# Kernel optimization log

Hardware: AMD Instinct MI355X
Metric: run time of the kernel (lower is better)

## Reference

```python
import jax, jax.numpy as jnp
import numpy as np

B, N, D = 64, 2048, 256
EPS = 1e-05


def setup_inputs() -> dict:
    key = jax.random.key(0)
    k1, k2 = jax.random.split(key)
    x = jax.random.normal(k1, (B, N, D), dtype=jnp.float32)
    lengths = jax.random.randint(k2, (B,), 1, N + 1, dtype=jnp.int32)
    weights = jnp.ones((D,), dtype=jnp.float32)
    biases = jnp.zeros((D,), dtype=jnp.float32)
    return {"x": x, "lengths": lengths, "weights": weights, "biases": biases}


def reference(x, lengths, weights, biases):
    # mask: [B, N, 1], 1.0 for valid set elements (idx < length)
    mask = (jnp.arange(N)[None, :] < lengths[:, None])[..., None].astype(x.dtype)
    denom = (lengths.astype(x.dtype) * D)  # [B]
    xm = x * mask
    means = jnp.sum(xm, axis=(1, 2)) / denom                      # [B]
    x_centered = (xm - means[:, None, None]) * mask               # [B,N,D]
    variances = jnp.sum(x_centered * x_centered, axis=(1, 2)) / denom  # [B]
    x_norm = x_centered / (jnp.sqrt(variances)[:, None, None] + EPS)
    # F.linear(x, diag_embed(w), b) == x * w + b (elementwise per-feature affine)
    out = (x_norm * weights + biases) * mask
    return out
```

## Files before the change

### kernel.cpp

```cpp
#include <hip/hip_runtime.h>


#define BB 64
#define NN 2048
#define DD 256
#define EPSV 1e-5f
#define CHUNKS 32
#define GROUPS (NN / 4)
#define BAT4 (NN * DD / 4)
#define K2_BPB 128

typedef float f32x4 __attribute__((ext_vector_type(4)));

__global__ __launch_bounds__(256) void setnorm_pass1(
    const float* __restrict__ x, const int* __restrict__ lengths,
    float* __restrict__ partials, float* __restrict__ out) {
  const int c = blockIdx.x;
  const int b = blockIdx.y;
  const int len = lengths[b];
  const int tRow = threadIdx.x >> 6;
  const f32x4* px = (const f32x4*)x + (size_t)b * BAT4;
  f32x4* po = (f32x4*)out + (size_t)b * BAT4;

  const int gFull = len >> 2;
  const int g4 = (len + 3) >> 2;
  int nFull = (gFull - c + 31) >> 5; if (nFull < 0) nFull = 0;
  int kZ = (g4 - c + 31) >> 5;       if (kZ < 0) kZ = 0;

  float sum = 0.f, sumsq = 0.f;
  #pragma unroll 4
  for (int k = 0; k < nFull; ++k) {
    const int g = c + (k << 5);
    const f32x4 v = px[g * 256 + threadIdx.x];
    sum += v.x + v.y + v.z + v.w;
    sumsq += v.x * v.x + v.y * v.y + v.z * v.z + v.w * v.w;
  }
  if ((len & 3) && ((gFull & 31) == c)) {
    const int idx = gFull * 256 + threadIdx.x;
    const int row = (gFull << 2) + tRow;
    if (row < len) {
      const f32x4 v = px[idx];
      sum += v.x + v.y + v.z + v.w;
      sumsq += v.x * v.x + v.y * v.y + v.z * v.z + v.w * v.w;
    } else {
      const f32x4 z = {0.f, 0.f, 0.f, 0.f};
      __builtin_nontemporal_store(z, po + idx);
    }
  }
  {
    const f32x4 z = {0.f, 0.f, 0.f, 0.f};
    #pragma unroll 4
    for (int k = kZ; k < 16; ++k) {
      const int g = c + (k << 5);
      __builtin_nontemporal_store(z, po + g * 256 + threadIdx.x);
    }
  }

  #pragma unroll
  for (int off = 32; off > 0; off >>= 1) {
    sum += __shfl_down(sum, off, 64);
    sumsq += __shfl_down(sumsq, off, 64);
  }
  __shared__ float ssum[4], ssq[4];
  const int wave = threadIdx.x >> 6;
  const int lane = threadIdx.x & 63;
  if (lane == 0) { ssum[wave] = sum; ssq[wave] = sumsq; }
  __syncthreads();
  if (threadIdx.x == 0) {
    const float ts = ssum[0] + ssum[1] + ssum[2] + ssum[3];
    const float tq = ssq[0] + ssq[1] + ssq[2] + ssq[3];
    partials[(b * CHUNKS + c) * 2 + 0] = ts;
    partials[(b * CHUNKS + c) * 2 + 1] = tq;
  }
}

__global__ __launch_bounds__(256) void setnorm_pass2(
    const float* __restrict__ x, const int* __restrict__ lengths,
    const float* __restrict__ weights, const float* __restrict__ biases,
    const float* __restrict__ partials, float* __restrict__ out) {
  const int blk = blockIdx.x;
  const int b = blk >> 7;
  const int j = blk & 127;
  const int len = lengths[b];
  if ((j << 2) >= len) return;

  __shared__ float s_mean, s_inv;
  if (threadIdx.x < 64) {
    float s = 0.f, q = 0.f;
    if (threadIdx.x < CHUNKS) {
      s = partials[(b * CHUNKS + threadIdx.x) * 2 + 0];
      q = partials[(b * CHUNKS + threadIdx.x) * 2 + 1];
    }
    #pragma unroll
    for (int off = 16; off > 0; off >>= 1) {
      s += __shfl_down(s, off, 64);
      q += __shfl_down(q, off, 64);
    }
    if (threadIdx.x == 0) {
      const float denom = (float)len * (float)DD;
      const float mean = s / denom;
      float var = q / denom - mean * mean;
      var = fmaxf(var, 0.f);
      s_mean = mean;
      s_inv = 1.f / (sqrtf(var) + EPSV);
    }
  }
  __syncthreads();
  const float mean = s_mean;
  const float inv = s_inv;

  const int d4 = threadIdx.x & 63;
  const f32x4 w = ((const f32x4*)weights)[d4];
  const f32x4 bi = ((const f32x4*)biases)[d4];
  const int tRow = threadIdx.x >> 6;

  const f32x4* px = (const f32x4*)x + (size_t)b * BAT4;
  f32x4* po = (f32x4*)out + (size_t)b * BAT4;
  #pragma unroll
  for (int i = 0; i < 4; ++i) {
    const int g = j + (i << 7);
    const int idx4 = g * 256 + threadIdx.x;
    const int row = (g << 2) + tRow;
    if (row < len) {
      const f32x4 v = px[idx4];
      f32x4 o;
      o.x = (v.x - mean) * inv * w.x + bi.x;
      o.y = (v.y - mean) * inv * w.y + bi.y;
      o.z = (v.z - mean) * inv * w.z + bi.z;
      o.w = (v.w - mean) * inv * w.w + bi.w;
      __builtin_nontemporal_store(o, po + idx4);
    }
  }
}

extern "C" void kernel_launch(void* const* d_in, const int* in_sizes, int n_in,
                              void* d_out, int out_size, void* d_ws, size_t ws_size,
                              hipStream_t stream) {
  const float* x = (const float*)d_in[0];
  const int* lengths = (const int*)d_in[1];
  const float* weights = (const float*)d_in[2];
  const float* biases = (const float*)d_in[3];
  float* out = (float*)d_out;

  float* partials = (float*)d_ws;

  dim3 g1(CHUNKS, BB);
  setnorm_pass1<<<g1, 256, 0, stream>>>(x, lengths, partials, out);
  setnorm_pass2<<<BB * K2_BPB, 256, 0, stream>>>(x, lengths, weights, biases,
                                                 partials, out);
}
```

Baseline: 232.4 us.

## Fuse two-pass set norm into one cooperative kernel with per-batch barrier

Replaces the separate statistics and normalize kernels with one cooperative kernel. Each block computes partial sums, signals a per-batch atomic counter, spins until all chunks of its batch finish, then normalizes the same chunk it just read. The aim is to remove the second launch and improve cache reuse of x between the passes. It adds a memset, a cooperative launch that requires all blocks to be co-resident, and spin-wait overhead. It falls back to the two-kernel path if the launch fails.

Result: slower. 472.0 us (+103.1%).

```diff
diff --git a/kernel.cpp b/kernel.cpp
--- a/kernel.cpp
+++ b/kernel.cpp
@@ -6,11 +6,132 @@
 #define DD 256
 #define EPSV 1e-5f
 #define CHUNKS 32
-#define GROUPS (NN / 4)
 #define BAT4 (NN * DD / 4)
-#define K2_BPB 128
+#define NBLOCKS (BB * CHUNKS)
 
 typedef float f32x4 __attribute__((ext_vector_type(4)));
+
+__global__ __launch_bounds__(256, 8) void setnorm_onepass(
+    const float* __restrict__ x, const int* __restrict__ lengths,
+    const float* __restrict__ weights, const float* __restrict__ biases,
+    float* __restrict__ partials, int* __restrict__ counters,
+    float* __restrict__ out) {
+  const int blk = blockIdx.x;
+  const int b = blk >> 5;
+  const int c = blk & 31;
+  const int len = lengths[b];
+  const int tRow = threadIdx.x >> 6;
+  const f32x4* px = (const f32x4*)x + (size_t)b * BAT4;
+  f32x4* po = (f32x4*)out + (size_t)b * BAT4;
+
+  const int gFull = len >> 2;
+  const int g4 = (len + 3) >> 2;
+  int nFull = (gFull - c + 31) >> 5; if (nFull < 0) nFull = 0;
+  int kZ = (g4 - c + 31) >> 5;       if (kZ < 0) kZ = 0;
+
+  float sum = 0.f, sumsq = 0.f;
+  #pragma unroll 4
+  for (int k = 0; k < nFull; ++k) {
+    const int g = c + (k << 5);
+    const f32x4 v = px[g * 256 + threadIdx.x];
+    sum += v.x + v.y + v.z + v.w;
+    sumsq += v.x * v.x + v.y * v.y + v.z * v.z + v.w * v.w;
+  }
+  if ((len & 3) && ((gFull & 31) == c)) {
+    const int idx = gFull * 256 + threadIdx.x;
+    const int row = (gFull << 2) + tRow;
+    if (row < len) {
+      const f32x4 v = px[idx];
+      sum += v.x + v.y + v.z + v.w;
+      sumsq += v.x * v.x + v.y * v.y + v.z * v.z + v.w * v.w;
+    } else {
+      const f32x4 z = {0.f, 0.f, 0.f, 0.f};
+      __builtin_nontemporal_store(z, po + idx);
+    }
+  }
+  #pragma unroll
+  for (int off = 32; off > 0; off >>= 1) {
+    sum += __shfl_down(sum, off, 64);
+    sumsq += __shfl_down(sumsq, off, 64);
+  }
+  __shared__ float ssum[4], ssq[4];
+  {
+    const int wave = threadIdx.x >> 6;
+    const int lane = threadIdx.x & 63;
+    if (lane == 0) { ssum[wave] = sum; ssq[wave] = sumsq; }
+  }
+  __syncthreads();
+  if (threadIdx.x == 0) {
+    partials[blk * 2 + 0] = ssum[0] + ssum[1] + ssum[2] + ssum[3];
+    partials[blk * 2 + 1] = ssq[0] + ssq[1] + ssq[2] + ssq[3];
+    __threadfence();
+    __hip_atomic_fetch_add(&counters[b], 1, __ATOMIC_ACQ_REL,
+                           __HIP_MEMORY_SCOPE_AGENT);
+  }
+
+  {
+    const f32x4 z = {0.f, 0.f, 0.f, 0.f};
+    #pragma unroll 4
+    for (int k = kZ; k < 16; ++k) {
+      const int g = c + (k << 5);
+      __builtin_nontemporal_store(z, po + g * 256 + threadIdx.x);
+    }
+  }
+  if (kZ == 0) return;
+
+  if (threadIdx.x == 0) {
+    while (__hip_atomic_load(&counters[b], __ATOMIC_ACQUIRE,
+                             __HIP_MEMORY_SCOPE_AGENT) != CHUNKS)
+      __builtin_amdgcn_s_sleep(8);
+  }
+  __syncthreads();
+
+  __shared__ float s_mean, s_inv;
+  if (threadIdx.x < 64) {
+    float s = 0.f, q = 0.f;
+    if (threadIdx.x < CHUNKS) {
+      s = __hip_atomic_load(&partials[(b * CHUNKS + threadIdx.x) * 2 + 0],
+                            __ATOMIC_RELAXED, __HIP_MEMORY_SCOPE_AGENT);
+      q = __hip_atomic_load(&partials[(b * CHUNKS + threadIdx.x) * 2 + 1],
+                            __ATOMIC_RELAXED, __HIP_MEMORY_SCOPE_AGENT);
+    }
+    #pragma unroll
+    for (int off = 16; off > 0; off >>= 1) {
+      s += __shfl_down(s, off, 64);
+      q += __shfl_down(q, off, 64);
+    }
+    if (threadIdx.x == 0) {
+      const float denom = (float)len * (float)DD;
+      const float mean = s / denom;
+      float var = q / denom - mean * mean;
+      var = fmaxf(var, 0.f);
+      s_mean = mean;
+      s_inv = 1.f / (sqrtf(var) + EPSV);
+    }
+  }
+  __syncthreads();
+  const float mean = s_mean;
+  const float inv = s_inv;
+
+  const int d4 = threadIdx.x & 63;
+  const f32x4 w = ((const f32x4*)weights)[d4];
+  const f32x4 bi = ((const f32x4*)biases)[d4];
+  #pragma unroll 4
+  for (int k = 0; k < kZ; ++k) {
+    const int g = c + (k << 5);
+    const int idx = g * 256 + threadIdx.x;
+    const int row = (g << 2) + tRow;
+    if (row < len) {
+      const f32x4 v = px[idx];
+      f32x4 o;
+      o.x = (v.x - mean) * inv * w.x + bi.x;
+      o.y = (v.y - mean) * inv * w.y + bi.y;
+      o.z = (v.z - mean) * inv * w.z + bi.z;
+      o.w = (v.w - mean) * inv * w.w + bi.w;
+      __builtin_nontemporal_store(o, po + idx);
+    }
+  }
+}
 
 __global__ __launch_bounds__(256) void setnorm_pass1(
     const float* __restrict__ x, const int* __restrict__ lengths,
@@ -55,7 +176,6 @@
       __builtin_nontemporal_store(z, po + g * 256 + threadIdx.x);
     }
   }
-
   #pragma unroll
   for (int off = 32; off > 0; off >>= 1) {
     sum += __shfl_down(sum, off, 64);
@@ -67,10 +187,8 @@
   if (lane == 0) { ssum[wave] = sum; ssq[wave] = sumsq; }
   __syncthreads();
   if (threadIdx.x == 0) {
-    const float ts = ssum[0] + ssum[1] + ssum[2] + ssum[3];
-    const float tq = ssq[0] + ssq[1] + ssq[2] + ssq[3];
-    partials[(b * CHUNKS + c) * 2 + 0] = ts;
-    partials[(b * CHUNKS + c) * 2 + 1] = tq;
+    partials[(b * CHUNKS + c) * 2 + 0] = ssum[0] + ssum[1] + ssum[2] + ssum[3];
+    partials[(b * CHUNKS + c) * 2 + 1] = ssq[0] + ssq[1] + ssq[2] + ssq[3];
   }
 }
 
@@ -143,9 +261,23 @@
   float* out = (float*)d_out;
 
   float* partials = (float*)d_ws;
-
+  int* counters = (int*)((char*)d_ws + BB * CHUNKS * 2 * sizeof(float));
+
+  bool fused_ok = ws_size >= (size_t)(BB * CHUNKS * 2 * sizeof(float) +
+                                      BB * sizeof(int));
+  if (fused_ok) {
+    hipError_t e = hipMemsetAsync(counters, 0, BB * sizeof(int), stream);
+    if (e == hipSuccess) {
+      void* args[] = {(void*)&x,        (void*)&lengths, (void*)&weights,
+                      (void*)&biases,   (void*)&partials, (void*)&counters,
+                      (void*)&out};
+      e = hipLaunchCooperativeKernel((const void*)setnorm_onepass,
+                                     dim3(NBLOCKS), dim3(256), args, 0, stream);
+    }
+    if (e == hipSuccess) return;
+  }
   dim3 g1(CHUNKS, BB);
   setnorm_pass1<<<g1, 256, 0, stream>>>(x, lengths, partials, out);
-  setnorm_pass2<<<BB * K2_BPB, 256, 0, stream>>>(x, lengths, weights, biases,
-                                                 partials, out);
-}
+  setnorm_pass2<<<BB * 128, 256, 0, stream>>>(x, lengths, weights, biases,
+                                              partials, out);
+}
```
